# Kernel tuning notes

Measured on AMD Instinct MI355X. Metric: run time of the kernel, lower is better.

## Reference

```python
import jax, jax.numpy as jnp
import numpy as np
from jax import lax

# Hyperparameters (match init_kwargs)
A = 0.9          # dynamic model: x_t = A * x_{t-1} + SIGMA * eps
SIGMA = 1.0
OBS_SIGMA = 1.0
LR = 0.1
ALPHA = 0.9
ITERATIONS = 3
EPS = 1e-8


def _pairwise_sq(x):
    # (B,N,N) squared euclidean distances ||x_i - x_j||^2
    x2 = jnp.sum(x * x, -1)
    sq = x2[:, :, None] + x2[:, None, :] - 2.0 * jnp.einsum('bid,bjd->bij', x, x)
    return jnp.maximum(sq, 0.0)


def _log_dynamic(x, prev):
    # logd[b,i,j] = log N(x_i ; A*prev_j, SIGMA^2 I)
    D = x.shape[-1]
    x2 = jnp.sum(x * x, -1)
    p2 = jnp.sum(prev * prev, -1)
    sq = x2[:, :, None] - 2.0 * A * jnp.einsum('bid,bjd->bij', x, prev) + (A * A) * p2[:, None, :]
    return -0.5 * sq / (SIGMA ** 2) - 0.5 * D * jnp.log(2.0 * jnp.pi * SIGMA ** 2)


def _post_grad(x, prev, obs):
    # softmax over j == max-subtract / exp / weighted-mean of d_log_dynamic in the original
    w = jax.nn.softmax(_log_dynamic(x, prev), axis=-1)                 # (B,N,N)
    mean_prev = jnp.einsum('bij,bjd->bid', w, prev)                    # sum_j w_ij * prev_j
    dyn_grad = -(x - A * mean_prev) / (SIGMA ** 2)                     # = sum_j w_ij * d_log_dynamic
    obs_grad = -(x - obs[:, None, :]) / (OBS_SIGMA ** 2)               # observation_model.d_score
    return dyn_grad + obs_grad


def _svgd(x, grad_fn):
    B, N, D = x.shape
    logN = jnp.log(jnp.asarray(N, x.dtype))
    step = jnp.zeros_like(x)
    for _ in range(ITERATIONS):
        sq = _pairwise_sq(x)                                           # (B,N,N)
        flat = jnp.sqrt(sq).reshape(B, N * N)
        med = jnp.sort(flat, axis=-1)[:, (N * N - 1) // 2]             # torch lower median of cdist
        h = (med * med / logN)[:, None, None]                          # (B,1,1) bandwidth
        rbf = jnp.exp(-sq / h)                                         # exp(-(1/h)*||x_i-x_j||^2)
        g = grad_fn(x)                                                 # (B,N,D) posterior score at particles
        kxy = jnp.einsum('bij,bjd->bid', rbf, g)                       # sum_j rbf_ij * g_j
        # sum_j d_rbf_ij = (2/h) * (x_i * sum_j rbf_ij - sum_j rbf_ij * x_j)   (avoids (B,N,N,D))
        rep = (2.0 / h) * (x * jnp.sum(rbf, -1)[..., None] - jnp.einsum('bij,bjd->bid', rbf, x))
        stein = (kxy + rep) / N
        step = ALPHA * step + (1.0 - ALPHA) * stein * stein            # RMSprop accumulator
        x = x + LR * stein / (jnp.sqrt(step) + EPS)
    return x


def setup_inputs() -> dict:
    key = jax.random.key(0)
    k1, k2, k3 = jax.random.split(key, 3)
    B, N, D = 8, 2048, 4
    return {
        'prev_state': jax.random.normal(k1, (B, N, D), jnp.float32),
        'observation': jax.random.normal(k2, (B, D), jnp.float32),
        'noise': jax.random.normal(k3, (B, N, D), jnp.float32),
    }


def reference(prev_state, observation, noise):
    N = prev_state.shape[1]
    logN = jnp.log(jnp.asarray(N, prev_state.dtype))
    # dynamic_model.sample
    state = A * prev_state + SIGMA * noise
    # post: logsumexp over i (dim=-2) of log_dynamic[b,i,j]
    log_post = jax.nn.logsumexp(_log_dynamic(state, prev_state), axis=1)   # (B,N)
    new_state = lax.stop_gradient(_svgd(state, lambda x: _post_grad(x, prev_state, observation)))
    log_weight = log_post - lax.stop_gradient(log_post) - logN             # value == -log N
    return jnp.concatenate([new_state, log_weight[..., None]], axis=-1)    # (B,N,D+1)
```

## Files before the change

### kernel.cpp

```cpp
#include <hip/hip_runtime.h>
#include <math.h>


#define NPART 2048
#define KRANK 2097151
#define LOGN_F 7.6246189861593985f
#define A_C 0.9f

__global__ __launch_bounds__(256) void k_init(const float* __restrict__ prev,
                                              const float* __restrict__ noise,
                                              float* __restrict__ x0,
                                              float* __restrict__ apb,
                                              int* __restrict__ hists) {
  int idx = blockIdx.x * 256 + threadIdx.x;
  float4 p  = ((const float4*)prev)[idx];
  float4 nz = ((const float4*)noise)[idx];
  float4 ap = make_float4(A_C*p.x, A_C*p.y, A_C*p.z, A_C*p.w);
  float4 x  = make_float4(ap.x+nz.x, ap.y+nz.y, ap.z+nz.z, ap.w+nz.w);
  ((float4*)x0)[idx]  = x;
  ((float4*)apb)[idx] = ap;
  ((int4*)hists)[idx] = make_int4(0, 0, 0, 0);
}

template <int PHASE>
__global__ __launch_bounds__(256) void k_hist(const float* __restrict__ x,
                                              const int* __restrict__ state,
                                              int* __restrict__ hist) {
  constexpr int NBIN = (PHASE == 0) ? 2048 : 4096;
  int b     = blockIdx.x >> 7;
  int sub   = blockIdx.x & 127;
  int itile = sub >> 4;
  int ktile = sub & 15;
  __shared__ float4 sxi[256];
  __shared__ float4 sxw[320];
  __shared__ int    sh[NBIN];

  const float4* xb = (const float4*)x + b*NPART;
  int ibase = itile*256;
  int k0 = ktile*64 + 1;
  sxi[threadIdx.x] = xb[ibase + threadIdx.x];
  for (int t = threadIdx.x; t < 320; t += 256)
    sxw[t] = xb[(ibase + k0 + t) & (NPART - 1)];
  for (int t = threadIdx.x; t < NBIN; t += 256) sh[t] = 0;
  int sel0 = (PHASE == 1) ? state[b*4 + 0] : 0;
  __syncthreads();

  float4 xi = sxi[threadIdx.x];
#pragma unroll 4
  for (int kk = 0; kk < 64; ++kk) {
    int w = (ktile == 15 && kk == 63) ? 1 : 2;
    float4 xj = sxw[threadIdx.x + kk];
    float dx = xi.x - xj.x, dy = xi.y - xj.y;
    float dz = xi.z - xj.z, dw = xi.w - xj.w;
    float sq = dx*dx + dy*dy + dz*dz + dw*dw;
    unsigned bits = __float_as_uint(sq);
    if (PHASE == 0) {
      atomicAdd(&sh[bits >> 20], w);
    } else {
      if ((int)(bits >> 20) == sel0) atomicAdd(&sh[(bits >> 8) & 4095], w);
    }
  }
  __syncthreads();
  int* hb = hist + b*NBIN;
  for (int t = threadIdx.x; t < NBIN; t += 256) {
    int c = sh[t];
    if (c) atomicAdd(&hb[t], c);
  }
}

__global__ __launch_bounds__(256) void k_scan0(const int* __restrict__ hist0,
                                               int* __restrict__ state) {
  int b = blockIdx.x;
  __shared__ int part[256];
  int s = 0;
  for (int c = 0; c < 8; ++c) s += hist0[b*2048 + threadIdx.x*8 + c];
  if (threadIdx.x == 0) s += NPART;
  part[threadIdx.x] = s;
  __syncthreads();
  if (threadIdx.x == 0) {
    int r = KRANK, cum = 0, ch = 0;
    for (; ch < 256; ++ch) { if (cum + part[ch] > r) break; cum += part[ch]; }
    int bin = ch * 8;
    for (;; ++bin) {
      int c = hist0[b*2048 + bin] + ((bin == 0) ? NPART : 0);
      if (cum + c > r) break;
      cum += c;
    }
    state[b*4 + 0] = bin;
    state[b*4 + 2] = r - cum;
  }
}

__global__ __launch_bounds__(256) void k_scan1(int* __restrict__ hist0,
                                               int* __restrict__ hist1,
                                               const int* __restrict__ state,
                                               float* __restrict__ hpar) {
  int b = blockIdx.x;
  __shared__ int part[256];
  int sel0 = state[b*4 + 0];
  int s = 0;
  for (int c = 0; c < 16; ++c) s += hist1[b*4096 + threadIdx.x*16 + c];
  if (threadIdx.x == 0 && sel0 == 0) s += NPART;
  part[threadIdx.x] = s;
  __syncthreads();
  if (threadIdx.x == 0) {
    int r = state[b*4 + 2], cum = 0, ch = 0;
    for (; ch < 256; ++ch) { if (cum + part[ch] > r) break; cum += part[ch]; }
    int bin = ch * 16;
    for (;; ++bin) {
      int c = hist1[b*4096 + bin] + ((sel0 == 0 && bin == 0) ? NPART : 0);
      if (cum + c > r) break;
      cum += c;
    }
    unsigned mb = (((unsigned)sel0) << 20) | (((unsigned)bin) << 8) | 128u;
    float med = sqrtf(__uint_as_float(mb));
    float h = med * med / LOGN_F;
    hpar[b*4 + 1] = -1.0f / h;
    hpar[b*4 + 2] = 2.0f / h;
  }
  __syncthreads();
  for (int t = threadIdx.x; t < 2048; t += 256) hist0[b*2048 + t] = 0;
  for (int t = threadIdx.x; t < 4096; t += 256) hist1[b*4096 + t] = 0;
}

__global__ __launch_bounds__(256) void k_grad(const float* __restrict__ x,
                                              const float* __restrict__ apb,
                                              const float* __restrict__ obs,
                                              float* __restrict__ g) {
  int b   = blockIdx.x >> 7;
  int ip  = threadIdx.x >> 4;
  int sub = threadIdx.x & 15;
  int i = (blockIdx.x & 127)*16 + ip;
  const float4* ab = (const float4*)apb + b*NPART;
  float4 xi = ((const float4*)x)[b*NPART + i];

  float sum1 = 0.f, sum2 = 0.f;
  float4 acc1 = make_float4(0.f,0.f,0.f,0.f);
  float4 acc2 = make_float4(0.f,0.f,0.f,0.f);
#pragma unroll 4
  for (int c = 0; c < 64; ++c) {
    int j = sub + 16*c;
    float4 a1 = ab[j];
    float4 a2 = ab[j + 1024];
    float dx1 = xi.x-a1.x, dy1 = xi.y-a1.y, dz1 = xi.z-a1.z, dw1 = xi.w-a1.w;
    float dx2 = xi.x-a2.x, dy2 = xi.y-a2.y, dz2 = xi.z-a2.z, dw2 = xi.w-a2.w;
    float e1 = __expf(-0.5f*(dx1*dx1 + dy1*dy1 + dz1*dz1 + dw1*dw1));
    float e2 = __expf(-0.5f*(dx2*dx2 + dy2*dy2 + dz2*dz2 + dw2*dw2));
    sum1 += e1; sum2 += e2;
    acc1.x += e1*a1.x; acc1.y += e1*a1.y; acc1.z += e1*a1.z; acc1.w += e1*a1.w;
    acc2.x += e2*a2.x; acc2.y += e2*a2.y; acc2.z += e2*a2.z; acc2.w += e2*a2.w;
  }
  float sum = sum1 + sum2;
  float4 acc = make_float4(acc1.x+acc2.x, acc1.y+acc2.y,
                           acc1.z+acc2.z, acc1.w+acc2.w);
#pragma unroll
  for (int d = 1; d < 16; d <<= 1) {
    sum   += __shfl_xor(sum, d);
    acc.x += __shfl_xor(acc.x, d);
    acc.y += __shfl_xor(acc.y, d);
    acc.z += __shfl_xor(acc.z, d);
    acc.w += __shfl_xor(acc.w, d);
  }
  if (sub == 0) {
    float inv = 1.0f / sum;
    float4 ob = ((const float4*)obs)[b];
    float4 gg;
    gg.x = acc.x*inv + ob.x - 2.0f*xi.x;
    gg.y = acc.y*inv + ob.y - 2.0f*xi.y;
    gg.z = acc.z*inv + ob.z - 2.0f*xi.z;
    gg.w = acc.w*inv + ob.w - 2.0f*xi.w;
    ((float4*)g)[b*NPART + i] = gg;
  }
}

template <int MODE>
__global__ __launch_bounds__(256) void k_stein(const float* __restrict__ x,
                                               const float* __restrict__ g,
                                               const float* __restrict__ hpar,
                                               float* __restrict__ stepb,
                                               float* __restrict__ xout,
                                               float* __restrict__ outp) {
  int b   = blockIdx.x >> 7;
  int ip  = threadIdx.x >> 4;
  int sub = threadIdx.x & 15;
  int i = (blockIdx.x & 127)*16 + ip;
  const float4* xb = (const float4*)x + b*NPART;
  const float4* gb = (const float4*)g + b*NPART;
  float neginvh = hpar[b*4 + 1];
  float two_h   = hpar[b*4 + 2];
  float4 xi = xb[i];

  float4 Sd1 = make_float4(0.f,0.f,0.f,0.f), Sd2 = Sd1;
  float4 Sg1 = Sd1, Sg2 = Sd1;
#pragma unroll 4
  for (int c = 0; c < 64; ++c) {
    int j = sub + 16*c;
    float4 xj1 = xb[j];
    float4 xj2 = xb[j + 1024];
    float4 gj1 = gb[j];
    float4 gj2 = gb[j + 1024];
    float dx1 = xi.x-xj1.x, dy1 = xi.y-xj1.y, dz1 = xi.z-xj1.z, dw1 = xi.w-xj1.w;
    float dx2 = xi.x-xj2.x, dy2 = xi.y-xj2.y, dz2 = xi.z-xj2.z, dw2 = xi.w-xj2.w;
    float e1 = __expf((dx1*dx1 + dy1*dy1 + dz1*dz1 + dw1*dw1) * neginvh);
    float e2 = __expf((dx2*dx2 + dy2*dy2 + dz2*dz2 + dw2*dw2) * neginvh);
    Sd1.x += e1*dx1; Sd1.y += e1*dy1; Sd1.z += e1*dz1; Sd1.w += e1*dw1;
    Sd2.x += e2*dx2; Sd2.y += e2*dy2; Sd2.z += e2*dz2; Sd2.w += e2*dw2;
    Sg1.x += e1*gj1.x; Sg1.y += e1*gj1.y; Sg1.z += e1*gj1.z; Sg1.w += e1*gj1.w;
    Sg2.x += e2*gj2.x; Sg2.y += e2*gj2.y; Sg2.z += e2*gj2.z; Sg2.w += e2*gj2.w;
  }
  float4 Sd = make_float4(Sd1.x+Sd2.x, Sd1.y+Sd2.y, Sd1.z+Sd2.z, Sd1.w+Sd2.w);
  float4 Sg = make_float4(Sg1.x+Sg2.x, Sg1.y+Sg2.y, Sg1.z+Sg2.z, Sg1.w+Sg2.w);
#pragma unroll
  for (int d = 1; d < 16; d <<= 1) {
    Sd.x += __shfl_xor(Sd.x, d); Sd.y += __shfl_xor(Sd.y, d);
    Sd.z += __shfl_xor(Sd.z, d); Sd.w += __shfl_xor(Sd.w, d);
    Sg.x += __shfl_xor(Sg.x, d); Sg.y += __shfl_xor(Sg.y, d);
    Sg.z += __shfl_xor(Sg.z, d); Sg.w += __shfl_xor(Sg.w, d);
  }
  if (sub == 0) {
    const float invN = 1.0f / 2048.0f;
    float4 sv;
    sv.x = (Sg.x + two_h*Sd.x) * invN;
    sv.y = (Sg.y + two_h*Sd.y) * invN;
    sv.z = (Sg.z + two_h*Sd.z) * invN;
    sv.w = (Sg.w + two_h*Sd.w) * invN;
    float4 st;
    if (MODE == 0) {
      st = make_float4(0.1f*sv.x*sv.x, 0.1f*sv.y*sv.y,
                       0.1f*sv.z*sv.z, 0.1f*sv.w*sv.w);
    } else {
      st = ((float4*)stepb)[b*NPART + i];
      st.x = 0.9f*st.x + 0.1f*sv.x*sv.x;
      st.y = 0.9f*st.y + 0.1f*sv.y*sv.y;
      st.z = 0.9f*st.z + 0.1f*sv.z*sv.z;
      st.w = 0.9f*st.w + 0.1f*sv.w*sv.w;
    }
    float4 xn;
    xn.x = xi.x + 0.1f*sv.x / (sqrtf(st.x) + 1e-8f);
    xn.y = xi.y + 0.1f*sv.y / (sqrtf(st.y) + 1e-8f);
    xn.z = xi.z + 0.1f*sv.z / (sqrtf(st.z) + 1e-8f);
    xn.w = xi.w + 0.1f*sv.w / (sqrtf(st.w) + 1e-8f);
    if (MODE != 2) {
      ((float4*)stepb)[b*NPART + i] = st;
      ((float4*)xout)[b*NPART + i] = xn;
    } else {
      float* o = outp + (size_t)(b*NPART + i) * 5;
      o[0] = xn.x; o[1] = xn.y; o[2] = xn.z; o[3] = xn.w;
      o[4] = -LOGN_F;
    }
  }
}

extern "C" void kernel_launch(void* const* d_in, const int* in_sizes, int n_in,
                              void* d_out, int out_size, void* d_ws, size_t ws_size,
                              hipStream_t stream) {
  const float* prev  = (const float*)d_in[0];
  const float* obs   = (const float*)d_in[1];
  const float* noise = (const float*)d_in[2];
  float* out = (float*)d_out;

  float* ws = (float*)d_ws;
  float* xA    = ws;
  float* xB    = xA + 65536;
  float* gbuf  = xB + 65536;
  float* stepb = gbuf + 65536;
  float* apb   = stepb + 65536;
  float* hpar  = apb + 65536;
  int*   state = (int*)(hpar + 32);
  int*   hist0 = state + 32;
  int*   hist1 = hist0 + 8*2048;

  k_init<<<64, 256, 0, stream>>>(prev, noise, xA, apb, hist0);

  float* xc = xA;
  float* xn = xB;
  for (int it = 0; it < 3; ++it) {
    k_grad<<<1024, 256, 0, stream>>>(xc, apb, obs, gbuf);
    k_hist<0><<<1024, 256, 0, stream>>>(xc, state, hist0);
    k_scan0<<<8, 256, 0, stream>>>(hist0, state);
    k_hist<1><<<1024, 256, 0, stream>>>(xc, state, hist1);
    k_scan1<<<8, 256, 0, stream>>>(hist0, hist1, state, hpar);
    if (it == 0) {
      k_stein<0><<<1024, 256, 0, stream>>>(xc, gbuf, hpar, stepb, xn, nullptr);
    } else if (it == 1) {
      k_stein<1><<<1024, 256, 0, stream>>>(xc, gbuf, hpar, stepb, xn, nullptr);
    } else {
      k_stein<2><<<1024, 256, 0, stream>>>(xc, gbuf, hpar, stepb, nullptr, out);
    }
    float* t = xc; xc = xn; xn = t;
  }
}
```

Baseline: 382.1 us.

## Fuse histogram scans into consumer kernels and merge grad with coarse histogram

Cuts each SVGD iteration from five launches to three. The gradient kernel and the coarse distance histogram now run as two halves of one grid. Each fine-histogram block recomputes the coarse median scan itself, and each Stein block recomputes the fine scan to get the bandwidth; histogram zeroing moves into the kernels that already run. The Stein kernel now handles two rows per thread, sharing the x_j and g_j loads, and the coarse shared histogram is split into two copies to reduce atomic contention. The cost is redundant per-block scan work and a less direct zeroing order that depends on the launch sequence.

```diff
diff --git a/kernel.cpp b/kernel.cpp
--- a/kernel.cpp
+++ b/kernel.cpp
@@ -11,29 +11,122 @@
                                               const float* __restrict__ noise,
                                               float* __restrict__ x0,
                                               float* __restrict__ apb,
-                                              int* __restrict__ hists) {
+                                              int* __restrict__ hist0) {
   int idx = blockIdx.x * 256 + threadIdx.x;
   float4 p  = ((const float4*)prev)[idx];
   float4 nz = ((const float4*)noise)[idx];
   float4 ap = make_float4(A_C*p.x, A_C*p.y, A_C*p.z, A_C*p.w);
-  float4 x  = make_float4(ap.x+nz.x, ap.y+nz.y, ap.z+nz.z, ap.w+nz.w);
-  ((float4*)x0)[idx]  = x;
+  ((float4*)x0)[idx]  = make_float4(ap.x+nz.x, ap.y+nz.y, ap.z+nz.z, ap.w+nz.w);
   ((float4*)apb)[idx] = ap;
-  ((int4*)hists)[idx] = make_int4(0, 0, 0, 0);
-}
-
-template <int PHASE>
-__global__ __launch_bounds__(256) void k_hist(const float* __restrict__ x,
-                                              const int* __restrict__ state,
-                                              int* __restrict__ hist) {
-  constexpr int NBIN = (PHASE == 0) ? 2048 : 4096;
+  if (idx < 4096) ((int4*)hist0)[idx] = make_int4(0, 0, 0, 0);
+}
+
+__global__ __launch_bounds__(256) void k_s1(const float* __restrict__ x,
+                                            const float* __restrict__ apb,
+                                            const float* __restrict__ obs,
+                                            float* __restrict__ g,
+                                            int* __restrict__ hist0,
+                                            int* __restrict__ hist1) {
+  if (threadIdx.x < 4)
+    ((int4*)hist1)[blockIdx.x*4 + threadIdx.x] = make_int4(0, 0, 0, 0);
+
+  if (blockIdx.x < 1024) {
+    int b   = blockIdx.x >> 7;
+    int ip  = threadIdx.x >> 4;
+    int sub = threadIdx.x & 15;
+    int i = (blockIdx.x & 127)*16 + ip;
+    const float4* ab = (const float4*)apb + b*NPART;
+    float4 xi = ((const float4*)x)[b*NPART + i];
+
+    float sum1 = 0.f, sum2 = 0.f;
+    float4 acc1 = make_float4(0.f,0.f,0.f,0.f);
+    float4 acc2 = make_float4(0.f,0.f,0.f,0.f);
+#pragma unroll 4
+    for (int c = 0; c < 64; ++c) {
+      int j = sub + 16*c;
+      float4 a1 = ab[j];
+      float4 a2 = ab[j + 1024];
+      float dx1 = xi.x-a1.x, dy1 = xi.y-a1.y, dz1 = xi.z-a1.z, dw1 = xi.w-a1.w;
+      float dx2 = xi.x-a2.x, dy2 = xi.y-a2.y, dz2 = xi.z-a2.z, dw2 = xi.w-a2.w;
+      float e1 = __expf(-0.5f*(dx1*dx1 + dy1*dy1 + dz1*dz1 + dw1*dw1));
+      float e2 = __expf(-0.5f*(dx2*dx2 + dy2*dy2 + dz2*dz2 + dw2*dw2));
+      sum1 += e1; sum2 += e2;
+      acc1.x += e1*a1.x; acc1.y += e1*a1.y; acc1.z += e1*a1.z; acc1.w += e1*a1.w;
+      acc2.x += e2*a2.x; acc2.y += e2*a2.y; acc2.z += e2*a2.z; acc2.w += e2*a2.w;
+    }
+    float sum = sum1 + sum2;
+    float4 acc = make_float4(acc1.x+acc2.x, acc1.y+acc2.y,
+                             acc1.z+acc2.z, acc1.w+acc2.w);
+#pragma unroll
+    for (int d = 1; d < 16; d <<= 1) {
+      sum   += __shfl_xor(sum, d);
+      acc.x += __shfl_xor(acc.x, d);
+      acc.y += __shfl_xor(acc.y, d);
+      acc.z += __shfl_xor(acc.z, d);
+      acc.w += __shfl_xor(acc.w, d);
+    }
+    if (sub == 0) {
+      float inv = 1.0f / sum;
+      float4 ob = ((const float4*)obs)[b];
+      float4 gg;
+      gg.x = acc.x*inv + ob.x - 2.0f*xi.x;
+      gg.y = acc.y*inv + ob.y - 2.0f*xi.y;
+      gg.z = acc.z*inv + ob.z - 2.0f*xi.z;
+      gg.w = acc.w*inv + ob.w - 2.0f*xi.w;
+      ((float4*)g)[b*NPART + i] = gg;
+    }
+  } else {
+    int bid   = blockIdx.x - 1024;
+    int b     = bid >> 7;
+    int sub2  = bid & 127;
+    int itile = sub2 >> 4;
+    int ktile = sub2 & 15;
+    __shared__ float4 sxi[256];
+    __shared__ float4 sxw[320];
+    __shared__ int    sh[2*2049];
+
+    const float4* xb = (const float4*)x + b*NPART;
+    int ibase = itile*256;
+    int k0 = ktile*64 + 1;
+    sxi[threadIdx.x] = xb[ibase + threadIdx.x];
+    for (int t = threadIdx.x; t < 320; t += 256)
+      sxw[t] = xb[(ibase + k0 + t) & (NPART - 1)];
+    for (int t = threadIdx.x; t < 2*2049; t += 256) sh[t] = 0;
+    __syncthreads();
+
+    float4 xi = sxi[threadIdx.x];
+    int cofs = (threadIdx.x & 1) * 2049;
+#pragma unroll 4
+    for (int kk = 0; kk < 64; ++kk) {
+      int w = (ktile == 15 && kk == 63) ? 1 : 2;
+      float4 xj = sxw[threadIdx.x + kk];
+      float dx = xi.x - xj.x, dy = xi.y - xj.y;
+      float dz = xi.z - xj.z, dw = xi.w - xj.w;
+      float sq = dx*dx + dy*dy + dz*dz + dw*dw;
+      atomicAdd(&sh[cofs + (__float_as_uint(sq) >> 20)], w);
+    }
+    __syncthreads();
+    int* hb = hist0 + b*2048;
+    for (int t = threadIdx.x; t < 2048; t += 256) {
+      int c = sh[t] + sh[t + 2049];
+      if (c) atomicAdd(&hb[t], c);
+    }
+  }
+}
+
+__global__ __launch_bounds__(256) void k_s2(const float* __restrict__ x,
+                                            int* __restrict__ state,
+                                            const int* __restrict__ hist0,
+                                            int* __restrict__ hist1) {
   int b     = blockIdx.x >> 7;
-  int sub   = blockIdx.x & 127;
-  int itile = sub >> 4;
-  int ktile = sub & 15;
+  int sub2  = blockIdx.x & 127;
+  int itile = sub2 >> 4;
+  int ktile = sub2 & 15;
   __shared__ float4 sxi[256];
   __shared__ float4 sxw[320];
-  __shared__ int    sh[NBIN];
+  __shared__ int    sh[4096];
+  __shared__ int    part[256];
+  __shared__ int    s_sel0;
 
   const float4* xb = (const float4*)x + b*NPART;
   int ibase = itile*256;
@@ -41,9 +134,30 @@
   sxi[threadIdx.x] = xb[ibase + threadIdx.x];
   for (int t = threadIdx.x; t < 320; t += 256)
     sxw[t] = xb[(ibase + k0 + t) & (NPART - 1)];
-  for (int t = threadIdx.x; t < NBIN; t += 256) sh[t] = 0;
-  int sel0 = (PHASE == 1) ? state[b*4 + 0] : 0;
-  __syncthreads();
+  for (int t = threadIdx.x; t < 4096; t += 256) sh[t] = 0;
+
+  const int* h0 = hist0 + b*2048;
+  int4 c0 = ((const int4*)h0)[threadIdx.x*2];
+  int4 c1 = ((const int4*)h0)[threadIdx.x*2 + 1];
+  int s = c0.x+c0.y+c0.z+c0.w + c1.x+c1.y+c1.z+c1.w;
+  if (threadIdx.x == 0) s += NPART;
+  part[threadIdx.x] = s;
+  __syncthreads();
+  if (threadIdx.x == 0) {
+    int r = KRANK, cum = 0, ch = 0;
+    for (; ch < 256; ++ch) { if (cum + part[ch] > r) break; cum += part[ch]; }
+    int4 d0 = ((const int4*)h0)[ch*2];
+    int4 d1 = ((const int4*)h0)[ch*2 + 1];
+    int cc[8] = {d0.x,d0.y,d0.z,d0.w,d1.x,d1.y,d1.z,d1.w};
+    if (ch == 0) cc[0] += NPART;
+    int q = 0;
+    for (;; ++q) { if (cum + cc[q] > r) break; cum += cc[q]; }
+    int bin = ch*8 + q;
+    s_sel0 = bin;
+    if (sub2 == 0) { state[b*2] = bin; state[b*2 + 1] = r - cum; }
+  }
+  __syncthreads();
+  int sel0 = s_sel0;
 
   float4 xi = sxi[threadIdx.x];
 #pragma unroll 4
@@ -54,199 +168,140 @@
     float dz = xi.z - xj.z, dw = xi.w - xj.w;
     float sq = dx*dx + dy*dy + dz*dz + dw*dw;
     unsigned bits = __float_as_uint(sq);
-    if (PHASE == 0) {
-      atomicAdd(&sh[bits >> 20], w);
-    } else {
-      if ((int)(bits >> 20) == sel0) atomicAdd(&sh[(bits >> 8) & 4095], w);
-    }
-  }
-  __syncthreads();
-  int* hb = hist + b*NBIN;
-  for (int t = threadIdx.x; t < NBIN; t += 256) {
+    if ((int)(bits >> 20) == sel0) atomicAdd(&sh[(bits >> 8) & 4095], w);
+  }
+  __syncthreads();
+  int* hb = hist1 + b*4096;
+  for (int t = threadIdx.x; t < 4096; t += 256) {
     int c = sh[t];
     if (c) atomicAdd(&hb[t], c);
   }
 }
 
-__global__ __launch_bounds__(256) void k_scan0(const int* __restrict__ hist0,
-                                               int* __restrict__ state) {
-  int b = blockIdx.x;
-  __shared__ int part[256];
-  int s = 0;
-  for (int c = 0; c < 8; ++c) s += hist0[b*2048 + threadIdx.x*8 + c];
-  if (threadIdx.x == 0) s += NPART;
-  part[threadIdx.x] = s;
-  __syncthreads();
-  if (threadIdx.x == 0) {
-    int r = KRANK, cum = 0, ch = 0;
-    for (; ch < 256; ++ch) { if (cum + part[ch] > r) break; cum += part[ch]; }
-    int bin = ch * 8;
-    for (;; ++bin) {
-      int c = hist0[b*2048 + bin] + ((bin == 0) ? NPART : 0);
-      if (cum + c > r) break;
-      cum += c;
-    }
-    state[b*4 + 0] = bin;
-    state[b*4 + 2] = r - cum;
-  }
-}
-
-__global__ __launch_bounds__(256) void k_scan1(int* __restrict__ hist0,
-                                               int* __restrict__ hist1,
-                                               const int* __restrict__ state,
-                                               float* __restrict__ hpar) {
-  int b = blockIdx.x;
-  __shared__ int part[256];
-  int sel0 = state[b*4 + 0];
-  int s = 0;
-  for (int c = 0; c < 16; ++c) s += hist1[b*4096 + threadIdx.x*16 + c];
+template <int MODE>
+__global__ __launch_bounds__(256) void k_s3(const float* __restrict__ x,
+                                            const float* __restrict__ g,
+                                            const int* __restrict__ state,
+                                            int* __restrict__ hist0,
+                                            const int* __restrict__ hist1,
+                                            float* __restrict__ stepb,
+                                            float* __restrict__ xout,
+                                            float* __restrict__ outp) {
+  if (threadIdx.x < 8)
+    ((int4*)hist0)[blockIdx.x*8 + threadIdx.x] = make_int4(0, 0, 0, 0);
+
+  int b   = blockIdx.x >> 6;
+  int blk = blockIdx.x & 63;
+  __shared__ int   part[256];
+  __shared__ float shp[2];
+
+  const int* h1 = hist1 + b*4096;
+  int4 c0 = ((const int4*)h1)[threadIdx.x*4 + 0];
+  int4 c1 = ((const int4*)h1)[threadIdx.x*4 + 1];
+  int4 c2 = ((const int4*)h1)[threadIdx.x*4 + 2];
+  int4 c3 = ((const int4*)h1)[threadIdx.x*4 + 3];
+  int s = c0.x+c0.y+c0.z+c0.w + c1.x+c1.y+c1.z+c1.w
+        + c2.x+c2.y+c2.z+c2.w + c3.x+c3.y+c3.z+c3.w;
+  int sel0 = state[b*2];
   if (threadIdx.x == 0 && sel0 == 0) s += NPART;
   part[threadIdx.x] = s;
   __syncthreads();
   if (threadIdx.x == 0) {
-    int r = state[b*4 + 2], cum = 0, ch = 0;
+    int r = state[b*2 + 1], cum = 0, ch = 0;
     for (; ch < 256; ++ch) { if (cum + part[ch] > r) break; cum += part[ch]; }
-    int bin = ch * 16;
-    for (;; ++bin) {
-      int c = hist1[b*4096 + bin] + ((sel0 == 0 && bin == 0) ? NPART : 0);
-      if (cum + c > r) break;
-      cum += c;
-    }
+    int4 d0 = ((const int4*)h1)[ch*4 + 0];
+    int4 d1 = ((const int4*)h1)[ch*4 + 1];
+    int4 d2 = ((const int4*)h1)[ch*4 + 2];
+    int4 d3 = ((const int4*)h1)[ch*4 + 3];
+    int cc[16] = {d0.x,d0.y,d0.z,d0.w, d1.x,d1.y,d1.z,d1.w,
+                  d2.x,d2.y,d2.z,d2.w, d3.x,d3.y,d3.z,d3.w};
+    if (sel0 == 0 && ch == 0) cc[0] += NPART;
+    int q = 0;
+    for (;; ++q) { if (cum + cc[q] > r) break; cum += cc[q]; }
+    int bin = ch*16 + q;
     unsigned mb = (((unsigned)sel0) << 20) | (((unsigned)bin) << 8) | 128u;
     float med = sqrtf(__uint_as_float(mb));
     float h = med * med / LOGN_F;
-    hpar[b*4 + 1] = -1.0f / h;
-    hpar[b*4 + 2] = 2.0f / h;
-  }
-  __syncthreads();
-  for (int t = threadIdx.x; t < 2048; t += 256) hist0[b*2048 + t] = 0;
-  for (int t = threadIdx.x; t < 4096; t += 256) hist1[b*4096 + t] = 0;
-}
-
-__global__ __launch_bounds__(256) void k_grad(const float* __restrict__ x,
-                                              const float* __restrict__ apb,
-                                              const float* __restrict__ obs,
-                                              float* __restrict__ g) {
-  int b   = blockIdx.x >> 7;
+    shp[0] = -1.0f / h;
+    shp[1] =  2.0f / h;
+  }
+  __syncthreads();
+  float neginvh = shp[0];
+  float two_h   = shp[1];
+
   int ip  = threadIdx.x >> 4;
   int sub = threadIdx.x & 15;
-  int i = (blockIdx.x & 127)*16 + ip;
-  const float4* ab = (const float4*)apb + b*NPART;
-  float4 xi = ((const float4*)x)[b*NPART + i];
-
-  float sum1 = 0.f, sum2 = 0.f;
-  float4 acc1 = make_float4(0.f,0.f,0.f,0.f);
-  float4 acc2 = make_float4(0.f,0.f,0.f,0.f);
+  int rowA = blk*32 + ip;
+  int rowB = rowA + 16;
+  const float4* xb = (const float4*)x + b*NPART;
+  const float4* gb = (const float4*)g + b*NPART;
+  float4 xiA = xb[rowA];
+  float4 xiB = xb[rowB];
+
+  float4 SdA = make_float4(0.f,0.f,0.f,0.f), SgA = SdA;
+  float4 SdB = SdA, SgB = SdA;
 #pragma unroll 4
-  for (int c = 0; c < 64; ++c) {
+  for (int c = 0; c < 128; ++c) {
     int j = sub + 16*c;
-    float4 a1 = ab[j];
-    float4 a2 = ab[j + 1024];
-    float dx1 = xi.x-a1.x, dy1 = xi.y-a1.y, dz1 = xi.z-a1.z, dw1 = xi.w-a1.w;
-    float dx2 = xi.x-a2.x, dy2 = xi.y-a2.y, dz2 = xi.z-a2.z, dw2 = xi.w-a2.w;
-    float e1 = __expf(-0.5f*(dx1*dx1 + dy1*dy1 + dz1*dz1 + dw1*dw1));
-    float e2 = __expf(-0.5f*(dx2*dx2 + dy2*dy2 + dz2*dz2 + dw2*dw2));
-    sum1 += e1; sum2 += e2;
-    acc1.x += e1*a1.x; acc1.y += e1*a1.y; acc1.z += e1*a1.z; acc1.w += e1*a1.w;
-    acc2.x += e2*a2.x; acc2.y += e2*a2.y; acc2.z += e2*a2.z; acc2.w += e2*a2.w;
-  }
-  float sum = sum1 + sum2;
-  float4 acc = make_float4(acc1.x+acc2.x, acc1.y+acc2.y,
-                           acc1.z+acc2.z, acc1.w+acc2.w);
+    float4 xj = xb[j];
+    float4 gj = gb[j];
+    float dxA = xiA.x-xj.x, dyA = xiA.y-xj.y, dzA = xiA.z-xj.z, dwA = xiA.w-xj.w;
+    float dxB = xiB.x-xj.x, dyB = xiB.y-xj.y, dzB = xiB.z-xj.z, dwB = xiB.w-xj.w;
+    float eA = __expf((dxA*dxA + dyA*dyA + dzA*dzA + dwA*dwA) * neginvh);
+    float eB = __expf((dxB*dxB + dyB*dyB + dzB*dzB + dwB*dwB) * neginvh);
+    SdA.x += eA*dxA; SdA.y += eA*dyA; SdA.z += eA*dzA; SdA.w += eA*dwA;
+    SdB.x += eB*dxB; SdB.y += eB*dyB; SdB.z += eB*dzB; SdB.w += eB*dwB;
+    SgA.x += eA*gj.x; SgA.y += eA*gj.y; SgA.z += eA*gj.z; SgA.w += eA*gj.w;
+    SgB.x += eB*gj.x; SgB.y += eB*gj.y; SgB.z += eB*gj.z; SgB.w += eB*gj.w;
+  }
 #pragma unroll
   for (int d = 1; d < 16; d <<= 1) {
-    sum   += __shfl_xor(sum, d);
-    acc.x += __shfl_xor(acc.x, d);
-    acc.y += __shfl_xor(acc.y, d);
-    acc.z += __shfl_xor(acc.z, d);
-    acc.w += __shfl_xor(acc.w, d);
-  }
-  if (sub == 0) {
-    float inv = 1.0f / sum;
-    float4 ob = ((const float4*)obs)[b];
-    float4 gg;
-    gg.x = acc.x*inv + ob.x - 2.0f*xi.x;
-    gg.y = acc.y*inv + ob.y - 2.0f*xi.y;
-    gg.z = acc.z*inv + ob.z - 2.0f*xi.z;
-    gg.w = acc.w*inv + ob.w - 2.0f*xi.w;
-    ((float4*)g)[b*NPART + i] = gg;
-  }
-}
-
-template <int MODE>
-__global__ __launch_bounds__(256) void k_stein(const float* __restrict__ x,
-                                               const float* __restrict__ g,
-                                               const float* __restrict__ hpar,
-                                               float* __restrict__ stepb,
-                                               float* __restrict__ xout,
-                                               float* __restrict__ outp) {
-  int b   = blockIdx.x >> 7;
-  int ip  = threadIdx.x >> 4;
-  int sub = threadIdx.x & 15;
-  int i = (blockIdx.x & 127)*16 + ip;
-  const float4* xb = (const float4*)x + b*NPART;
-  const float4* gb = (const float4*)g + b*NPART;
-  float neginvh = hpar[b*4 + 1];
-  float two_h   = hpar[b*4 + 2];
-  float4 xi = xb[i];
-
-  float4 Sd1 = make_float4(0.f,0.f,0.f,0.f), Sd2 = Sd1;
-  float4 Sg1 = Sd1, Sg2 = Sd1;
-#pragma unroll 4
-  for (int c = 0; c < 64; ++c) {
-    int j = sub + 16*c;
-    float4 xj1 = xb[j];
-    float4 xj2 = xb[j + 1024];
-    float4 gj1 = gb[j];
-    float4 gj2 = gb[j + 1024];
-    float dx1 = xi.x-xj1.x, dy1 = xi.y-xj1.y, dz1 = xi.z-xj1.z, dw1 = xi.w-xj1.w;
-    float dx2 = xi.x-xj2.x, dy2 = xi.y-xj2.y, dz2 = xi.z-xj2.z, dw2 = xi.w-xj2.w;
-    float e1 = __expf((dx1*dx1 + dy1*dy1 + dz1*dz1 + dw1*dw1) * neginvh);
-    float e2 = __expf((dx2*dx2 + dy2*dy2 + dz2*dz2 + dw2*dw2) * neginvh);
-    Sd1.x += e1*dx1; Sd1.y += e1*dy1; Sd1.z += e1*dz1; Sd1.w += e1*dw1;
-    Sd2.x += e2*dx2; Sd2.y += e2*dy2; Sd2.z += e2*dz2; Sd2.w += e2*dw2;
-    Sg1.x += e1*gj1.x; Sg1.y += e1*gj1.y; Sg1.z += e1*gj1.z; Sg1.w += e1*gj1.w;
-    Sg2.x += e2*gj2.x; Sg2.y += e2*gj2.y; Sg2.z += e2*gj2.z; Sg2.w += e2*gj2.w;
-  }
-  float4 Sd = make_float4(Sd1.x+Sd2.x, Sd1.y+Sd2.y, Sd1.z+Sd2.z, Sd1.w+Sd2.w);
-  float4 Sg = make_float4(Sg1.x+Sg2.x, Sg1.y+Sg2.y, Sg1.z+Sg2.z, Sg1.w+Sg2.w);
-#pragma unroll
-  for (int d = 1; d < 16; d <<= 1) {
-    Sd.x += __shfl_xor(Sd.x, d); Sd.y += __shfl_xor(Sd.y, d);
-    Sd.z += __shfl_xor(Sd.z, d); Sd.w += __shfl_xor(Sd.w, d);
-    Sg.x += __shfl_xor(Sg.x, d); Sg.y += __shfl_xor(Sg.y, d);
-    Sg.z += __shfl_xor(Sg.z, d); Sg.w += __shfl_xor(Sg.w, d);
+    SdA.x += __shfl_xor(SdA.x, d); SdA.y += __shfl_xor(SdA.y, d);
+    SdA.z += __shfl_xor(SdA.z, d); SdA.w += __shfl_xor(SdA.w, d);
+    SgA.x += __shfl_xor(SgA.x, d); SgA.y += __shfl_xor(SgA.y, d);
+    SgA.z += __shfl_xor(SgA.z, d); SgA.w += __shfl_xor(SgA.w, d);
+    SdB.x += __shfl_xor(SdB.x, d); SdB.y += __shfl_xor(SdB.y, d);
+    SdB.z += __shfl_xor(SdB.z, d); SdB.w += __shfl_xor(SdB.w, d);
+    SgB.x += __shfl_xor(SgB.x, d); SgB.y += __shfl_xor(SgB.y, d);
+    SgB.z += __shfl_xor(SgB.z, d); SgB.w += __shfl_xor(SgB.w, d);
   }
   if (sub == 0) {
     const float invN = 1.0f / 2048.0f;
-    float4 sv;
-    sv.x = (Sg.x + two_h*Sd.x) * invN;
-    sv.y = (Sg.y + two_h*Sd.y) * invN;
-    sv.z = (Sg.z + two_h*Sd.z) * invN;
-    sv.w = (Sg.w + two_h*Sd.w) * invN;
-    float4 st;
-    if (MODE == 0) {
-      st = make_float4(0.1f*sv.x*sv.x, 0.1f*sv.y*sv.y,
-                       0.1f*sv.z*sv.z, 0.1f*sv.w*sv.w);
-    } else {
-      st = ((float4*)stepb)[b*NPART + i];
-      st.x = 0.9f*st.x + 0.1f*sv.x*sv.x;
-      st.y = 0.9f*st.y + 0.1f*sv.y*sv.y;
-      st.z = 0.9f*st.z + 0.1f*sv.z*sv.z;
-      st.w = 0.9f*st.w + 0.1f*sv.w*sv.w;
-    }
-    float4 xn;
-    xn.x = xi.x + 0.1f*sv.x / (sqrtf(st.x) + 1e-8f);
-    xn.y = xi.y + 0.1f*sv.y / (sqrtf(st.y) + 1e-8f);
-    xn.z = xi.z + 0.1f*sv.z / (sqrtf(st.z) + 1e-8f);
-    xn.w = xi.w + 0.1f*sv.w / (sqrtf(st.w) + 1e-8f);
-    if (MODE != 2) {
-      ((float4*)stepb)[b*NPART + i] = st;
-      ((float4*)xout)[b*NPART + i] = xn;
-    } else {
-      float* o = outp + (size_t)(b*NPART + i) * 5;
-      o[0] = xn.x; o[1] = xn.y; o[2] = xn.z; o[3] = xn.w;
-      o[4] = -LOGN_F;
+#pragma unroll
+    for (int rr = 0; rr < 2; ++rr) {
+      int row = rr ? rowB : rowA;
+      float4 xi = rr ? xiB : xiA;
+      float4 Sd = rr ? SdB : SdA;
+      float4 Sg = rr ? SgB : SgA;
+      float4 sv;
+      sv.x = (Sg.x + two_h*Sd.x) * invN;
+      sv.y = (Sg.y + two_h*Sd.y) * invN;
+      sv.z = (Sg.z + two_h*Sd.z) * invN;
+      sv.w = (Sg.w + two_h*Sd.w) * invN;
+      float4 st;
+      if (MODE == 0) {
+        st = make_float4(0.1f*sv.x*sv.x, 0.1f*sv.y*sv.y,
+                         0.1f*sv.z*sv.z, 0.1f*sv.w*sv.w);
+      } else {
+        st = ((float4*)stepb)[b*NPART + row];
+        st.x = 0.9f*st.x + 0.1f*sv.x*sv.x;
+        st.y = 0.9f*st.y + 0.1f*sv.y*sv.y;
+        st.z = 0.9f*st.z + 0.1f*sv.z*sv.z;
+        st.w = 0.9f*st.w + 0.1f*sv.w*sv.w;
+      }
+      float4 xn;
+      xn.x = xi.x + 0.1f*sv.x / (sqrtf(st.x) + 1e-8f);
+      xn.y = xi.y + 0.1f*sv.y / (sqrtf(st.y) + 1e-8f);
+      xn.z = xi.z + 0.1f*sv.z / (sqrtf(st.z) + 1e-8f);
+      xn.w = xi.w + 0.1f*sv.w / (sqrtf(st.w) + 1e-8f);
+      if (MODE != 2) {
+        ((float4*)stepb)[b*NPART + row] = st;
+        ((float4*)xout)[b*NPART + row] = xn;
+      } else {
+        float* o = outp + (size_t)(b*NPART + row) * 5;
+        o[0] = xn.x; o[1] = xn.y; o[2] = xn.z; o[3] = xn.w;
+        o[4] = -LOGN_F;
+      }
     }
   }
 }
@@ -265,9 +320,8 @@
   float* gbuf  = xB + 65536;
   float* stepb = gbuf + 65536;
   float* apb   = stepb + 65536;
-  float* hpar  = apb + 65536;
-  int*   state = (int*)(hpar + 32);
-  int*   hist0 = state + 32;
+  int*   state = (int*)(apb + 65536);
+  int*   hist0 = state + 16;
   int*   hist1 = hist0 + 8*2048;
 
   k_init<<<64, 256, 0, stream>>>(prev, noise, xA, apb, hist0);
@@ -275,17 +329,14 @@
   float* xc = xA;
   float* xn = xB;
   for (int it = 0; it < 3; ++it) {
-    k_grad<<<1024, 256, 0, stream>>>(xc, apb, obs, gbuf);
-    k_hist<0><<<1024, 256, 0, stream>>>(xc, state, hist0);
-    k_scan0<<<8, 256, 0, stream>>>(hist0, state);
-    k_hist<1><<<1024, 256, 0, stream>>>(xc, state, hist1);
-    k_scan1<<<8, 256, 0, stream>>>(hist0, hist1, state, hpar);
+    k_s1<<<2048, 256, 0, stream>>>(xc, apb, obs, gbuf, hist0, hist1);
+    k_s2<<<1024, 256, 0, stream>>>(xc, state, hist0, hist1);
     if (it == 0) {
-      k_stein<0><<<1024, 256, 0, stream>>>(xc, gbuf, hpar, stepb, xn, nullptr);
+      k_s3<0><<<512, 256, 0, stream>>>(xc, gbuf, state, hist0, hist1, stepb, xn, nullptr);
     } else if (it == 1) {
-      k_stein<1><<<1024, 256, 0, stream>>>(xc, gbuf, hpar, stepb, xn, nullptr);
+      k_s3<1><<<512, 256, 0, stream>>>(xc, gbuf, state, hist0, hist1, stepb, xn, nullptr);
     } else {
-      k_stein<2><<<1024, 256, 0, stream>>>(xc, gbuf, hpar, stepb, nullptr, out);
+      k_s3<2><<<512, 256, 0, stream>>>(xc, gbuf, state, hist0, hist1, stepb, nullptr, out);
     }
     float* t = xc; xc = xn; xn = t;
   }
```

Result: faster. 359.5 us (-5.9%).
